# Optimization experiments

Hardware: AMD Instinct MI355X
Metric: run time of the kernel (lower is better)

## Reference

```python
import jax, jax.numpy as jnp
import numpy as np

N = 128          # number of samples; P = N*(N-1)/2 = 8128 pairs
D = 8128         # feature dim; must equal P for the module's einsum('ij,ji->i')
EPS = 1e-12

# static pair indices matching the original loop order: for i, for j < i
_II, _JJ = np.tril_indices(N, k=-1)  # each length P = 8128


def setup_inputs() -> dict:
    key = jax.random.key(0)
    k1, k2 = jax.random.split(key)
    S_real = jax.random.normal(k1, (N, D), dtype=jnp.float32)
    S_fake = jax.random.normal(k2, (N, D), dtype=jnp.float32)
    return {"S_real": S_real, "S_fake": S_fake}


def _cosine_loss(real, fake, eps):
    # real, fake: [P, D] with P == D
    norm_real = jnp.linalg.norm(real, axis=1, keepdims=True)
    norm_fake = jnp.linalg.norm(fake, axis=1, keepdims=True)
    mat_real = jnp.maximum(real / norm_real, eps)
    mat_fake = jnp.maximum(fake / norm_fake, eps)
    # einsum('ij,ji->i') then sum == total sum of mat_fake * mat_real.T
    return jnp.einsum('ij,ji->i', mat_fake, mat_real).sum()


def reference(S_real, S_fake):
    # vectorized pairwise differences, same order as the python double loop
    v_real = S_real[_II] - S_real[_JJ]   # [P, D]
    v_fake = S_fake[_II] - S_fake[_JJ]   # [P, D]
    return _cosine_loss(v_real, v_fake, EPS)
```

## Files before the change

kernel.cpp:

```cpp
#include <hip/hip_runtime.h>

#define NS   128
#define D_   8128
#define DP_  8192
#define P_   8128
#define PP   8192
#define EPSV 1e-12f
#define NT   127
#define KS8  8

typedef __attribute__((ext_vector_type(8))) short short8;
typedef __attribute__((ext_vector_type(4))) float f32x4;

static __device__ __forceinline__ unsigned short f32_to_bf16_rne(float f) {
    unsigned int u = __float_as_uint(f);
    return (unsigned short)((u + 0x7fffu + ((u >> 16) & 1u)) >> 16);
}
static __device__ __forceinline__ unsigned int pack2_bf16(float a, float b) {
    return (unsigned int)f32_to_bf16_rne(a) | ((unsigned int)f32_to_bf16_rne(b) << 16);
}
static __device__ __forceinline__ float bf16_lo(unsigned int u) { return __uint_as_float(u << 16); }
static __device__ __forceinline__ float bf16_hi(unsigned int u) { return __uint_as_float(u & 0xffff0000u); }

static __device__ __forceinline__ f32x4 gen4(uint2 a, uint2 b, float inv) {
    f32x4 r;
    r.x = fmaxf((bf16_lo(a.x) - bf16_lo(b.x)) * inv, EPSV);
    r.y = fmaxf((bf16_hi(a.x) - bf16_hi(b.x)) * inv, EPSV);
    r.z = fmaxf((bf16_lo(a.y) - bf16_lo(b.y)) * inv, EPSV);
    r.w = fmaxf((bf16_hi(a.y) - bf16_hi(b.y)) * inv, EPSV);
    return r;
}

__global__ void cvt_pad(const float* __restrict__ Sr, const float* __restrict__ Sf,
                        unsigned short* __restrict__ Sr16, unsigned short* __restrict__ Sf16) {
    int idx = blockIdx.x * 256 + threadIdx.x;
    int m   = idx >> 17;
    int rem = idx & 131071;
    int row = rem >> 10;
    int c8  = rem & 1023;
    const float* __restrict__ S = m ? Sf : Sr;
    unsigned short* __restrict__ Dst = m ? Sf16 : Sr16;
    uint4 o;
    if (c8 < 1016) {
        const float* src = S + (size_t)row * D_ + 8 * c8;
        float4 v0 = *(const float4*)src;
        float4 v1 = *(const float4*)(src + 4);
        o.x = pack2_bf16(v0.x, v0.y);
        o.y = pack2_bf16(v0.z, v0.w);
        o.z = pack2_bf16(v1.x, v1.y);
        o.w = pack2_bf16(v1.z, v1.w);
    } else {
        o.x = 0u; o.y = 0u; o.z = 0u; o.w = 0u;
    }
    *(uint4*)(Dst + (size_t)row * DP_ + 8 * c8) = o;
}

__global__ void __launch_bounds__(64)
gram_direct(const unsigned short* __restrict__ Sr16, const unsigned short* __restrict__ Sf16,
            float* __restrict__ Gpart8) {
    int tile = blockIdx.x;
    int I = tile >> 3, J = tile & 7;
    int m = blockIdx.y;
    int s = blockIdx.z;
    const unsigned short* __restrict__ S = m ? Sf16 : Sr16;
    float* __restrict__ out = Gpart8 + ((size_t)s * 2 + m) * (NS * NS);

    int l  = threadIdx.x;
    int lr = l & 15;
    int kf = (l >> 4) * 8;

    const unsigned short* pa = S + (size_t)(I * 16 + lr) * DP_ + kf;
    const unsigned short* pb = S + (size_t)(J * 16 + lr) * DP_ + kf;

    f32x4 acc = (f32x4)0.f;
    int ks0 = s * 32;
    int ks1 = (ks0 + 32 < 254) ? ks0 + 32 : 254;
    #pragma unroll 4
    for (int ks = ks0; ks < ks1; ++ks) {
        short8 a = *(const short8*)(pa + ks * 32);
        short8 b = *(const short8*)(pb + ks * 32);
        acc = __builtin_amdgcn_mfma_f32_16x16x32_bf16(a, b, acc, 0, 0, 0);
    }
    int rbase = I * 16 + (l >> 4) * 4;
    int col   = J * 16 + lr;
    #pragma unroll
    for (int r = 0; r < 4; ++r)
        out[(rbase + r) * NS + col] = acc[r];
}

__global__ void norm_finish(const float* __restrict__ Gpart8,
                            float* __restrict__ inv_nr, float* __restrict__ inv_nf,
                            int* __restrict__ opi, int* __restrict__ opj) {
    int p = blockIdx.x * 256 + threadIdx.x;
    if (p >= PP) return;
    if (p >= P_) {
        inv_nr[p] = 0.f;
        inv_nf[p] = 0.f;
        opi[p] = 0;
        opj[p] = 0;
        return;
    }
    int i = (int)((1.0f + sqrtf(8.0f * (float)p + 1.0f)) * 0.5f);
    while (i * (i - 1) / 2 > p) --i;
    while ((i + 1) * i / 2 <= p) ++i;
    int j = p - i * (i - 1) / 2;

    float rii = 0.f, rjj = 0.f, rij = 0.f;
    float fii = 0.f, fjj = 0.f, fij = 0.f;
    #pragma unroll
    for (int s = 0; s < KS8; ++s) {
        const float* g0 = Gpart8 + ((size_t)s * 2 + 0) * (NS * NS);
        const float* g1 = Gpart8 + ((size_t)s * 2 + 1) * (NS * NS);
        rii += g0[i * NS + i]; rjj += g0[j * NS + j]; rij += g0[i * NS + j];
        fii += g1[i * NS + i]; fjj += g1[j * NS + j]; fij += g1[i * NS + j];
    }
    inv_nr[p] = rsqrtf(fmaxf(rii + rjj - 2.f * rij, 1e-30f));
    inv_nf[p] = rsqrtf(fmaxf(fii + fjj - 2.f * fij, 1e-30f));
    opi[p] = i * DP_;
    opj[p] = j * DP_;
}

__global__ void __launch_bounds__(256, 6)
tile10_kernel(const unsigned short* __restrict__ Sr16, const unsigned short* __restrict__ Sf16,
              const float* __restrict__ inv_nr, const float* __restrict__ inv_nf,
              const int* __restrict__ opi, const int* __restrict__ opj,
              float* __restrict__ partials) {
    __shared__ unsigned short Sfl[128 * 64];
    __shared__ float wsum[4];

    int t  = threadIdx.x;
    int q0 = blockIdx.y * 64;
    int pg = t & 15;
    int qg = t >> 4;

    #pragma unroll
    for (int s = 0; s < 8; ++s) {
        int task = t + 256 * s;
        int row = task >> 4, slot = task & 15;
        uint2 v = *(const uint2*)(Sf16 + (size_t)row * DP_ + q0 + 4 * slot);
        *(uint2*)&Sfl[row * 64 + 4 * (slot ^ (row & 15))] = v;
    }

    int q4 = q0 + 4 * qg;
    int4   oiq   = *(const int4*)&opi[q4];
    int4   ojq   = *(const int4*)&opj[q4];
    float4 invr4 = *(const float4*)&inv_nr[q4];
    __syncthreads();

    float acc = 0.f;
    for (int step = 0; step < 8; ++step) {
        int pb = ((blockIdx.x * 8 + step) << 6) + 4 * pg;

        int4   pio   = *(const int4*)&opi[pb];
        int4   pjo   = *(const int4*)&opj[pb];
        float4 invf4 = *(const float4*)&inv_nf[pb];

        uint2 ru0 = *(const uint2*)(Sr16 + oiq.x + pb);
        uint2 rv0 = *(const uint2*)(Sr16 + ojq.x + pb);
        uint2 ru1 = *(const uint2*)(Sr16 + oiq.y + pb);
        uint2 rv1 = *(const uint2*)(Sr16 + ojq.y + pb);
        uint2 ru2 = *(const uint2*)(Sr16 + oiq.z + pb);
        uint2 rv2 = *(const uint2*)(Sr16 + ojq.z + pb);
        uint2 ru3 = *(const uint2*)(Sr16 + oiq.w + pb);
        uint2 rv3 = *(const uint2*)(Sr16 + ojq.w + pb);

        int ii0 = pio.x >> 13, jj0 = pjo.x >> 13;
        int ii1 = pio.y >> 13, jj1 = pjo.y >> 13;
        int ii2 = pio.z >> 13, jj2 = pjo.z >> 13;
        int ii3 = pio.w >> 13, jj3 = pjo.w >> 13;
        uint2 fu0 = *(const uint2*)&Sfl[ii0 * 64 + 4 * (qg ^ (ii0 & 15))];
        uint2 fv0 = *(const uint2*)&Sfl[jj0 * 64 + 4 * (qg ^ (jj0 & 15))];
        uint2 fu1 = *(const uint2*)&Sfl[ii1 * 64 + 4 * (qg ^ (ii1 & 15))];
        uint2 fv1 = *(const uint2*)&Sfl[jj1 * 64 + 4 * (qg ^ (jj1 & 15))];
        uint2 fu2 = *(const uint2*)&Sfl[ii2 * 64 + 4 * (qg ^ (ii2 & 15))];
        uint2 fv2 = *(const uint2*)&Sfl[jj2 * 64 + 4 * (qg ^ (jj2 & 15))];
        uint2 fu3 = *(const uint2*)&Sfl[ii3 * 64 + 4 * (qg ^ (ii3 & 15))];
        uint2 fv3 = *(const uint2*)&Sfl[jj3 * 64 + 4 * (qg ^ (jj3 & 15))];

        f32x4 R0 = gen4(ru0, rv0, invr4.x);
        f32x4 R1 = gen4(ru1, rv1, invr4.y);
        f32x4 R2 = gen4(ru2, rv2, invr4.z);
        f32x4 R3 = gen4(ru3, rv3, invr4.w);
        f32x4 F0 = gen4(fu0, fv0, invf4.x);
        f32x4 F1 = gen4(fu1, fv1, invf4.y);
        f32x4 F2 = gen4(fu2, fv2, invf4.z);
        f32x4 F3 = gen4(fu3, fv3, invf4.w);

        acc += F0.x * R0.x + F0.y * R1.x + F0.z * R2.x + F0.w * R3.x;
        acc += F1.x * R0.y + F1.y * R1.y + F1.z * R2.y + F1.w * R3.y;
        acc += F2.x * R0.z + F2.y * R1.z + F2.z * R2.z + F2.w * R3.z;
        acc += F3.x * R0.w + F3.y * R1.w + F3.z * R2.w + F3.w * R3.w;
    }

    #pragma unroll
    for (int off = 32; off > 0; off >>= 1) acc += __shfl_down(acc, off, 64);
    if ((t & 63) == 0) wsum[t >> 6] = acc;
    __syncthreads();
    if (t == 0) partials[blockIdx.y * 16 + blockIdx.x] = wsum[0] + wsum[1] + wsum[2] + wsum[3];
}

__global__ void norms_kernel(const float* __restrict__ Sr, const float* __restrict__ Sf,
                             float* __restrict__ inv_nr, float* __restrict__ inv_nf,
                             int* __restrict__ opi, int* __restrict__ opj) {
    int p = blockIdx.x;
    int i = (int)((1.0f + sqrtf(8.0f * (float)p + 1.0f)) * 0.5f);
    while (i * (i - 1) / 2 > p) --i;
    while ((i + 1) * i / 2 <= p) ++i;
    int j = p - i * (i - 1) / 2;

    const float4* ri = (const float4*)(Sr + (size_t)i * D_);
    const float4* rj = (const float4*)(Sr + (size_t)j * D_);
    const float4* fi = (const float4*)(Sf + (size_t)i * D_);
    const float4* fj = (const float4*)(Sf + (size_t)j * D_);

    float sr = 0.f, sf = 0.f;
    for (int d = threadIdx.x; d < D_ / 4; d += 256) {
        float4 a = ri[d], b = rj[d];
        float dx = a.x - b.x, dy = a.y - b.y, dz = a.z - b.z, dw = a.w - b.w;
        sr += dx * dx + dy * dy + dz * dz + dw * dw;
        float4 c2 = fi[d], e = fj[d];
        dx = c2.x - e.x; dy = c2.y - e.y; dz = c2.z - e.z; dw = c2.w - e.w;
        sf += dx * dx + dy * dy + dz * dz + dw * dw;
    }
    #pragma unroll
    for (int off = 32; off > 0; off >>= 1) {
        sr += __shfl_down(sr, off, 64);
        sf += __shfl_down(sf, off, 64);
    }
    __shared__ float wr[4], wf[4];
    int wave = threadIdx.x >> 6;
    if ((threadIdx.x & 63) == 0) { wr[wave] = sr; wf[wave] = sf; }
    __syncthreads();
    if (threadIdx.x == 0) {
        inv_nr[p] = 1.0f / sqrtf(wr[0] + wr[1] + wr[2] + wr[3]);
        inv_nf[p] = 1.0f / sqrtf(wf[0] + wf[1] + wf[2] + wf[3]);
        opi[p] = i * D_;
        opj[p] = j * D_;
    }
}

__global__ void __launch_bounds__(256, 6)
tile3_kernel(const float* __restrict__ Sr, const float* __restrict__ Sf,
             const float* __restrict__ inv_nr, const float* __restrict__ inv_nf,
             const int* __restrict__ opi, const int* __restrict__ opj,
             float* __restrict__ partials) {
    __shared__ float Rt[64][65];
    __shared__ int   sIp[64], sJp[64];
    __shared__ float sInvF[64];
    __shared__ float wsum[4];

    int t  = threadIdx.x;
    int p0 = blockIdx.x * 64, q0 = blockIdx.y * 64;

    if (t < 64) {
        int p = p0 + t;
        sIp[t]   = opi[p];
        sJp[t]   = opj[p];
        sInvF[t] = inv_nf[p];
    }
    {
        int c  = t & 15;
        int qr = t >> 4;
        #pragma unroll
        for (int pass = 0; pass < 4; ++pass) {
            int qq = qr + 16 * pass;
            int q  = q0 + qq;
            int oi = opi[q], oj = opj[q];
            float invr = inv_nr[q];
            const float4 a = *(const float4*)(Sr + oi + p0 + 4 * c);
            const float4 b = *(const float4*)(Sr + oj + p0 + 4 * c);
            Rt[4 * c + 0][qq] = fmaxf((a.x - b.x) * invr, EPSV);
            Rt[4 * c + 1][qq] = fmaxf((a.y - b.y) * invr, EPSV);
            Rt[4 * c + 2][qq] = fmaxf((a.z - b.z) * invr, EPSV);
            Rt[4 * c + 3][qq] = fmaxf((a.w - b.w) * invr, EPSV);
        }
    }
    __syncthreads();

    int qg = t & 15;
    int pg = t >> 4;
    float ax = 0.f, ay = 0.f, az = 0.f, aw = 0.f;
    #pragma unroll
    for (int pp = 0; pp < 4; ++pp) {
        int prow = pg + 16 * pp;
        int oi = sIp[prow], oj = sJp[prow];
        float invf = sInvF[prow];
        const float4 fa = *(const float4*)(Sf + oi + q0 + 4 * qg);
        const float4 fb = *(const float4*)(Sf + oj + q0 + 4 * qg);
        const float4 r  = *(const float4*)&Rt[prow][4 * qg];
        ax += fmaxf((fa.x - fb.x) * invf, EPSV) * r.x;
        ay += fmaxf((fa.y - fb.y) * invf, EPSV) * r.y;
        az += fmaxf((fa.z - fb.z) * invf, EPSV) * r.z;
        aw += fmaxf((fa.w - fb.w) * invf, EPSV) * r.w;
    }
    float acc = (ax + ay) + (az + aw);

    #pragma unroll
    for (int off = 32; off > 0; off >>= 1) acc += __shfl_down(acc, off, 64);
    int w = t >> 6;
    if ((t & 63) == 0) wsum[w] = acc;
    __syncthreads();
    if (t == 0) partials[blockIdx.y * NT + blockIdx.x] = wsum[0] + wsum[1] + wsum[2] + wsum[3];
}

__global__ void reduce_kernel(const float* __restrict__ partials, int n, float* __restrict__ out) {
    float s = 0.f;
    for (int idx = threadIdx.x; idx < n; idx += 1024) s += partials[idx];
    #pragma unroll
    for (int off = 32; off > 0; off >>= 1) s += __shfl_down(s, off, 64);
    __shared__ float wbuf[16];
    int wave = threadIdx.x >> 6;
    if ((threadIdx.x & 63) == 0) wbuf[wave] = s;
    __syncthreads();
    if (threadIdx.x == 0) {
        float tot = 0.f;
        #pragma unroll
        for (int k = 0; k < 16; ++k) tot += wbuf[k];
        out[0] = tot;
    }
}

extern "C" void kernel_launch(void* const* d_in, const int* in_sizes, int n_in,
                              void* d_out, int out_size, void* d_ws, size_t ws_size,
                              hipStream_t stream) {
    const float* Sr = (const float*)d_in[0];
    const float* Sf = (const float*)d_in[1];
    float* out = (float*)d_out;

    char* w = (char*)d_ws;
    unsigned short* Sr16 = (unsigned short*)w;   w += (size_t)NS * DP_ * 2;
    unsigned short* Sf16 = (unsigned short*)w;   w += (size_t)NS * DP_ * 2;
    float* inv_nr = (float*)w;                   w += (size_t)PP * 4;
    float* inv_nf = (float*)w;                   w += (size_t)PP * 4;
    int*   opi    = (int*)w;                     w += (size_t)PP * 4;
    int*   opj    = (int*)w;                     w += (size_t)PP * 4;
    float* tpart  = (float*)w;                   w += (size_t)16384 * 4;
    float* Gpart8 = (float*)w;                   w += (size_t)KS8 * 2 * NS * NS * 4;
    size_t need = (size_t)(w - (char*)d_ws);

    if (ws_size >= need) {
        cvt_pad<<<1024, 256, 0, stream>>>(Sr, Sf, Sr16, Sf16);
        dim3 gg(64, 2, KS8);
        gram_direct<<<gg, 64, 0, stream>>>(Sr16, Sf16, Gpart8);
        norm_finish<<<32, 256, 0, stream>>>(Gpart8, inv_nr, inv_nf, opi, opj);
        dim3 grid(16, 128);
        tile10_kernel<<<grid, 256, 0, stream>>>(Sr16, Sf16, inv_nr, inv_nf, opi, opj, tpart);
        reduce_kernel<<<1, 1024, 0, stream>>>(tpart, 2048, out);
    } else {
        norms_kernel<<<P_, 256, 0, stream>>>(Sr, Sf, inv_nr, inv_nf, opi, opj);
        dim3 grid(NT, NT);
        tile3_kernel<<<grid, 256, 0, stream>>>(Sr, Sf, inv_nr, inv_nf, opi, opj, tpart);
        reduce_kernel<<<1, 1024, 0, stream>>>(tpart, NT * NT, out);
    }
}
```

Baseline: 54.74 us.

## Fuse bf16 conversion into LDS-tiled Gram kernel and fold final reduction

The separate fp32-to-bf16 conversion kernel is merged into the Gram-matrix kernel. Each of 64 blocks stages a 128x32 bf16 slice in shared memory, writes the bf16 copy to global memory, and computes a full 128x128 partial Gram over its K-slice with MFMA. The final reduce kernel is replaced by a last-block-done pattern: an atomic counter, reset in norm_finish, lets the last tile block sum the partials. This removes two launches and redundant global reads, in exchange for more Gram partials to sum in norm_finish, fewer Gram blocks, and extra atomic/fence overhead.

```diff
diff --git a/kernel.cpp b/kernel.cpp
--- a/kernel.cpp
+++ b/kernel.cpp
@@ -7,7 +7,8 @@
 #define PP   8192
 #define EPSV 1e-12f
 #define NT   127
-#define KS8  8
+#define KS32 32
+#define TNB  2048
 
 typedef __attribute__((ext_vector_type(8))) short short8;
 typedef __attribute__((ext_vector_type(4))) float f32x4;
@@ -15,9 +16,6 @@
 static __device__ __forceinline__ unsigned short f32_to_bf16_rne(float f) {
     unsigned int u = __float_as_uint(f);
     return (unsigned short)((u + 0x7fffu + ((u >> 16) & 1u)) >> 16);
-}
-static __device__ __forceinline__ unsigned int pack2_bf16(float a, float b) {
-    return (unsigned int)f32_to_bf16_rne(a) | ((unsigned int)f32_to_bf16_rne(b) << 16);
 }
 static __device__ __forceinline__ float bf16_lo(unsigned int u) { return __uint_as_float(u << 16); }
 static __device__ __forceinline__ float bf16_hi(unsigned int u) { return __uint_as_float(u & 0xffff0000u); }
@@ -31,67 +29,90 @@
     return r;
 }
 
-__global__ void cvt_pad(const float* __restrict__ Sr, const float* __restrict__ Sf,
-                        unsigned short* __restrict__ Sr16, unsigned short* __restrict__ Sf16) {
-    int idx = blockIdx.x * 256 + threadIdx.x;
-    int m   = idx >> 17;
-    int rem = idx & 131071;
-    int row = rem >> 10;
-    int c8  = rem & 1023;
+__global__ void __launch_bounds__(256)
+gram_cvt(const float* __restrict__ Sr, const float* __restrict__ Sf,
+         unsigned short* __restrict__ Sr16, unsigned short* __restrict__ Sf16,
+         float* __restrict__ Gpart) {
+    int sl = blockIdx.x;
+    int m  = blockIdx.y;
     const float* __restrict__ S = m ? Sf : Sr;
-    unsigned short* __restrict__ Dst = m ? Sf16 : Sr16;
-    uint4 o;
-    if (c8 < 1016) {
-        const float* src = S + (size_t)row * D_ + 8 * c8;
-        float4 v0 = *(const float4*)src;
-        float4 v1 = *(const float4*)(src + 4);
-        o.x = pack2_bf16(v0.x, v0.y);
-        o.y = pack2_bf16(v0.z, v0.w);
-        o.z = pack2_bf16(v1.x, v1.y);
-        o.w = pack2_bf16(v1.z, v1.w);
-    } else {
-        o.x = 0u; o.y = 0u; o.z = 0u; o.w = 0u;
-    }
-    *(uint4*)(Dst + (size_t)row * DP_ + 8 * c8) = o;
-}
-
-__global__ void __launch_bounds__(64)
-gram_direct(const unsigned short* __restrict__ Sr16, const unsigned short* __restrict__ Sf16,
-            float* __restrict__ Gpart8) {
-    int tile = blockIdx.x;
-    int I = tile >> 3, J = tile & 7;
-    int m = blockIdx.y;
-    int s = blockIdx.z;
-    const unsigned short* __restrict__ S = m ? Sf16 : Sr16;
-    float* __restrict__ out = Gpart8 + ((size_t)s * 2 + m) * (NS * NS);
-
-    int l  = threadIdx.x;
+    unsigned short* __restrict__ S16 = m ? Sf16 : Sr16;
+    float* __restrict__ out = Gpart + ((size_t)sl * 2 + m) * (NS * NS);
+
+    __shared__ short St[128 * 40];
+
+    int t = threadIdx.x;
+    int w = t >> 6, l = t & 63;
     int lr = l & 15;
     int kf = (l >> 4) * 8;
 
-    const unsigned short* pa = S + (size_t)(I * 16 + lr) * DP_ + kf;
-    const unsigned short* pb = S + (size_t)(J * 16 + lr) * DP_ + kf;
-
-    f32x4 acc = (f32x4)0.f;
-    int ks0 = s * 32;
-    int ks1 = (ks0 + 32 < 254) ? ks0 + 32 : 254;
-    #pragma unroll 4
+    int ks0 = sl * 8;
+    int ks1 = (ks0 + 8 < 254) ? ks0 + 8 : 254;
+
+    f32x4 acc[2][8];
+    #pragma unroll
+    for (int fr = 0; fr < 2; ++fr)
+        #pragma unroll
+        for (int c = 0; c < 8; ++c) acc[fr][c] = (f32x4)0.f;
+
     for (int ks = ks0; ks < ks1; ++ks) {
-        short8 a = *(const short8*)(pa + ks * 32);
-        short8 b = *(const short8*)(pb + ks * 32);
-        acc = __builtin_amdgcn_mfma_f32_16x16x32_bf16(a, b, acc, 0, 0, 0);
-    }
-    int rbase = I * 16 + (l >> 4) * 4;
-    int col   = J * 16 + lr;
-    #pragma unroll
-    for (int r = 0; r < 4; ++r)
-        out[(rbase + r) * NS + col] = acc[r];
-}
-
-__global__ void norm_finish(const float* __restrict__ Gpart8,
+        int k0 = ks * 32;
+        #pragma unroll
+        for (int g4 = 0; g4 < 4; ++g4) {
+            int task = t + 256 * g4;
+            int row  = task >> 3;
+            int g    = task & 7;
+            float4 v = *(const float4*)(S + (size_t)row * D_ + k0 + 4 * g);
+            ushort4 o;
+            o.x = f32_to_bf16_rne(v.x);
+            o.y = f32_to_bf16_rne(v.y);
+            o.z = f32_to_bf16_rne(v.z);
+            o.w = f32_to_bf16_rne(v.w);
+            *(ushort4*)&St[row * 40 + 4 * g] = o;
+            *(ushort4*)(S16 + (size_t)row * DP_ + k0 + 4 * g) = o;
+        }
+        __syncthreads();
+
+        short8 a0 = *(const short8*)&St[(w * 32 + lr) * 40 + kf];
+        short8 a1 = *(const short8*)&St[(w * 32 + 16 + lr) * 40 + kf];
+        #pragma unroll
+        for (int c = 0; c < 8; ++c) {
+            short8 b = *(const short8*)&St[(c * 16 + lr) * 40 + kf];
+            acc[0][c] = __builtin_amdgcn_mfma_f32_16x16x32_bf16(a0, b, acc[0][c], 0, 0, 0);
+            acc[1][c] = __builtin_amdgcn_mfma_f32_16x16x32_bf16(a1, b, acc[1][c], 0, 0, 0);
+        }
+        __syncthreads();
+    }
+
+    if (sl == KS32 - 1) {
+        #pragma unroll
+        for (int g = 0; g < 4; ++g) {
+            int idx = t + 256 * g;
+            int row = idx >> 3, c4 = idx & 7;
+            uint4 z; z.x = 0u; z.y = 0u; z.z = 0u; z.w = 0u;
+            *(uint4*)(S16 + (size_t)row * DP_ + D_ + 8 * c4) = z;
+        }
+    }
+
+    #pragma unroll
+    for (int fr = 0; fr < 2; ++fr) {
+        int rbase = w * 32 + fr * 16 + (l >> 4) * 4;
+        #pragma unroll
+        for (int c = 0; c < 8; ++c) {
+            int col = c * 16 + lr;
+            #pragma unroll
+            for (int r = 0; r < 4; ++r)
+                out[(rbase + r) * NS + col] = acc[fr][c][r];
+        }
+    }
+}
+
+__global__ void norm_finish(const float* __restrict__ Gpart,
                             float* __restrict__ inv_nr, float* __restrict__ inv_nf,
-                            int* __restrict__ opi, int* __restrict__ opj) {
+                            int* __restrict__ opi, int* __restrict__ opj,
+                            unsigned int* __restrict__ dcount) {
     int p = blockIdx.x * 256 + threadIdx.x;
+    if (p == 0) *dcount = 0u;
     if (p >= PP) return;
     if (p >= P_) {
         inv_nr[p] = 0.f;
@@ -107,10 +128,10 @@
 
     float rii = 0.f, rjj = 0.f, rij = 0.f;
     float fii = 0.f, fjj = 0.f, fij = 0.f;
-    #pragma unroll
-    for (int s = 0; s < KS8; ++s) {
-        const float* g0 = Gpart8 + ((size_t)s * 2 + 0) * (NS * NS);
-        const float* g1 = Gpart8 + ((size_t)s * 2 + 1) * (NS * NS);
+    #pragma unroll 4
+    for (int s = 0; s < KS32; ++s) {
+        const float* g0 = Gpart + ((size_t)s * 2 + 0) * (NS * NS);
+        const float* g1 = Gpart + ((size_t)s * 2 + 1) * (NS * NS);
         rii += g0[i * NS + i]; rjj += g0[j * NS + j]; rij += g0[i * NS + j];
         fii += g1[i * NS + i]; fjj += g1[j * NS + j]; fij += g1[i * NS + j];
     }
@@ -121,12 +142,15 @@
 }
 
 __global__ void __launch_bounds__(256, 6)
-tile10_kernel(const unsigned short* __restrict__ Sr16, const unsigned short* __restrict__ Sf16,
+tile11_kernel(const unsigned short* __restrict__ Sr16, const unsigned short* __restrict__ Sf16,
               const float* __restrict__ inv_nr, const float* __restrict__ inv_nf,
               const int* __restrict__ opi, const int* __restrict__ opj,
-              float* __restrict__ partials) {
+              float* __restrict__ partials, unsigned int* __restrict__ dcount,
+              float* __restrict__ out) {
     __shared__ unsigned short Sfl[128 * 64];
     __shared__ float wsum[4];
+    __shared__ float wsum2[4];
+    __shared__ int lastFlag;
 
     int t  = threadIdx.x;
     int q0 = blockIdx.y * 64;
@@ -196,7 +220,27 @@
     for (int off = 32; off > 0; off >>= 1) acc += __shfl_down(acc, off, 64);
     if ((t & 63) == 0) wsum[t >> 6] = acc;
     __syncthreads();
-    if (t == 0) partials[blockIdx.y * 16 + blockIdx.x] = wsum[0] + wsum[1] + wsum[2] + wsum[3];
+
+    if (t == 0) {
+        float tot = wsum[0] + wsum[1] + wsum[2] + wsum[3];
+        partials[blockIdx.y * 16 + blockIdx.x] = tot;
+        __threadfence();
+        unsigned int prev = atomicAdd(dcount, 1u);
+        lastFlag = (prev == TNB - 1) ? 1 : 0;
+    }
+    __syncthreads();
+    if (lastFlag) {
+        __threadfence();
+        float s = 0.f;
+        #pragma unroll
+        for (int k = 0; k < TNB / 256; ++k)
+            s += partials[t + 256 * k];
+        #pragma unroll
+        for (int off = 32; off > 0; off >>= 1) s += __shfl_down(s, off, 64);
+        if ((t & 63) == 0) wsum2[t >> 6] = s;
+        __syncthreads();
+        if (t == 0) out[0] = wsum2[0] + wsum2[1] + wsum2[2] + wsum2[3];
+    }
 }
 
 __global__ void norms_kernel(const float* __restrict__ Sr, const float* __restrict__ Sf,
@@ -335,17 +379,17 @@
     int*   opi    = (int*)w;                     w += (size_t)PP * 4;
     int*   opj    = (int*)w;                     w += (size_t)PP * 4;
     float* tpart  = (float*)w;                   w += (size_t)16384 * 4;
-    float* Gpart8 = (float*)w;                   w += (size_t)KS8 * 2 * NS * NS * 4;
+    float* Gpart  = (float*)w;                   w += (size_t)KS32 * 2 * NS * NS * 4;
+    unsigned int* dcount = (unsigned int*)w;     w += 16;
     size_t need = (size_t)(w - (char*)d_ws);
 
     if (ws_size >= need) {
-        cvt_pad<<<1024, 256, 0, stream>>>(Sr, Sf, Sr16, Sf16);
-        dim3 gg(64, 2, KS8);
-        gram_direct<<<gg, 64, 0, stream>>>(Sr16, Sf16, Gpart8);
-        norm_finish<<<32, 256, 0, stream>>>(Gpart8, inv_nr, inv_nf, opi, opj);
+        dim3 gg(KS32, 2);
+        gram_cvt<<<gg, 256, 0, stream>>>(Sr, Sf, Sr16, Sf16, Gpart);
+        norm_finish<<<32, 256, 0, stream>>>(Gpart, inv_nr, inv_nf, opi, opj, dcount);
         dim3 grid(16, 128);
-        tile10_kernel<<<grid, 256, 0, stream>>>(Sr16, Sf16, inv_nr, inv_nf, opi, opj, tpart);
-        reduce_kernel<<<1, 1024, 0, stream>>>(tpart, 2048, out);
+        tile11_kernel<<<grid, 256, 0, stream>>>(Sr16, Sf16, inv_nr, inv_nf, opi, opj,
+                                                tpart, dcount, out);
     } else {
         norms_kernel<<<P_, 256, 0, stream>>>(Sr, Sf, inv_nr, inv_nf, opi, opj);
         dim3 grid(NT, NT);
```

After: 97.99 us. 79.0% more time.
